# Performance work log

Measured on AMD Instinct MI355X. Metric: run time of the kernel, lower is better.

The kernel has to match this reference:

```python
import jax, jax.numpy as jnp
import numpy as np

D, H, DFF, K, S = 512, 8, 2048, 4, 4
DH = D // H
SHAPES = [(56, 56), (28, 28), (14, 14), (7, 7)]
B = 4


def setup_inputs() -> dict:
    key = jax.random.key(0)
    ks = jax.random.split(key, 32)
    inp = {}
    for i, (hl, wl) in enumerate(SHAPES):
        inp[f'src{i}'] = jax.random.normal(ks[i], (B, hl, wl, D), jnp.float32)
        inp[f'ref{i}'] = jax.random.uniform(ks[4 + i], (B, hl, wl, 2), jnp.float32)
    def lin(k, fan_in, fan_out):
        return jax.random.normal(k, (fan_in, fan_out), jnp.float32) * (1.0 / np.sqrt(fan_in))
    inp['Wv'] = lin(ks[8], D, D)
    inp['bv'] = jnp.zeros((D,), jnp.float32)
    inp['Woff'] = jax.random.normal(ks[9], (D, H * S * K * 2), jnp.float32) * 0.01
    inp['boff'] = jax.random.normal(ks[10], (H * S * K * 2,), jnp.float32) * 0.1
    inp['Wattn'] = jax.random.normal(ks[11], (D, H * S * K), jnp.float32) * 0.01
    inp['battn'] = jnp.zeros((H * S * K,), jnp.float32)
    inp['Wo'] = lin(ks[12], D, D)
    inp['bo'] = jnp.zeros((D,), jnp.float32)
    inp['W1'] = lin(ks[13], D, DFF)
    inp['b1'] = jnp.zeros((DFF,), jnp.float32)
    inp['W2'] = lin(ks[14], DFF, D)
    inp['b2'] = jnp.zeros((D,), jnp.float32)
    inp['g1'] = jnp.ones((D,), jnp.float32)
    inp['be1'] = jnp.zeros((D,), jnp.float32)
    inp['g2'] = jnp.ones((D,), jnp.float32)
    inp['be2'] = jnp.zeros((D,), jnp.float32)
    return inp


def layernorm(x, g, b, eps=1e-5):
    mu = jnp.mean(x, axis=-1, keepdims=True)
    var = jnp.mean(jnp.square(x - mu), axis=-1, keepdims=True)
    return (x - mu) * jax.lax.rsqrt(var + eps) * g + b


def bilinear_sample(value, loc):
    # value: [B, Hl, Wl, H, DH] per-scale projected values; loc: [B, Lq, H, K, 2] in [0,1]
    b, hl, wl, h, dh = value.shape
    x = loc[..., 0] * wl - 0.5
    y = loc[..., 1] * hl - 0.5
    x0f = jnp.floor(x); y0f = jnp.floor(y)
    wx1 = x - x0f; wx0 = 1.0 - wx1
    wy1 = y - y0f; wy0 = 1.0 - wy1
    x0 = x0f.astype(jnp.int32); y0 = y0f.astype(jnp.int32)
    vflat = value.transpose(0, 3, 1, 2, 4).reshape(b, h, hl * wl, dh)  # [B,H,HW,DH]

    def corner(xi, yi, w):
        valid = ((xi >= 0) & (xi < wl) & (yi >= 0) & (yi < hl)).astype(value.dtype)
        idx = jnp.clip(yi, 0, hl - 1) * wl + jnp.clip(xi, 0, wl - 1)  # [B,Lq,H,K]
        idx = idx.transpose(0, 2, 1, 3)  # [B,H,Lq,K]
        lq, kk = idx.shape[2], idx.shape[3]
        g = jnp.take_along_axis(vflat, idx.reshape(b, h, lq * kk)[..., None], axis=2)
        g = g.reshape(b, h, lq, kk, dh)
        wv = (w * valid).transpose(0, 2, 1, 3)[..., None]  # [B,H,Lq,K,1]
        return g * wv

    out = (corner(x0, y0, wx0 * wy0) + corner(x0 + 1, y0, wx1 * wy0)
           + corner(x0, y0 + 1, wx0 * wy1) + corner(x0 + 1, y0 + 1, wx1 * wy1))
    return out.transpose(0, 2, 1, 3, 4)  # [B,Lq,H,K,DH]


def _forward(src0, src1, src2, src3, ref0, ref1, ref2, ref3,
             Wv, bv, Woff, boff, Wattn, battn, Wo, bo, W1, b1, W2, b2, g1, be1, g2, be2):
    srcs = [src0, src1, src2, src3]
    refs = [ref0, ref1, ref2, ref3]
    # shared value projection per scale, split into heads
    values = [(s @ Wv + bv).reshape(s.shape[0], s.shape[1], s.shape[2], H, DH) for s in srcs]
    outs = []
    for src_l, ref_l in zip(srcs, refs):
        b = src_l.shape[0]
        q = src_l.reshape(b, -1, D)          # [B,Lq,D]
        ref = ref_l.reshape(b, -1, 2)        # [B,Lq,2]
        lq = q.shape[1]
        off = (q @ Woff + boff).reshape(b, lq, H, S, K, 2)
        attn = jax.nn.softmax((q @ Wattn + battn).reshape(b, lq, H, S * K), axis=-1)
        attn = attn.reshape(b, lq, H, S, K)
        acc = jnp.zeros((b, lq, H, DH), q.dtype)
        for li, (v, (hl, wl)) in enumerate(zip(values, SHAPES)):
            scale = jnp.array([wl, hl], q.dtype)
            loc = ref[:, :, None, None, :] + off[:, :, :, li] / scale  # [B,Lq,H,K,2]
            samp = bilinear_sample(v, loc)                              # [B,Lq,H,K,DH]
            acc = acc + jnp.einsum('blhk,blhkd->blhd', attn[:, :, :, li], samp)
        a = acc.reshape(b, lq, D) @ Wo + bo
        x = layernorm(q + a, g1, be1)
        f = jax.nn.relu(x @ W1 + b1) @ W2 + b2
        x = layernorm(x + f, g2, be2)
        outs.append(x)
    return jnp.concatenate(outs, axis=1)  # [B, sum(Hl*Wl), D]


def reference(src0, src1, src2, src3, ref0, ref1, ref2, ref3,
              Wv, bv, Woff, boff, Wattn, battn, Wo, bo, W1, b1, W2, b2, g1, be1, g2, be2):
    return _forward(src0, src1, src2, src3, ref0, ref1, ref2, ref3,
                    Wv, bv, Woff, boff, Wattn, battn, Wo, bo, W1, b1, W2, b2, g1, be1, g2, be2)
```

## Files before the change

### kernel.cpp

```cpp
#include <hip/hip_runtime.h>
#include <math.h>


#define TTOT 16660
#define TPAD 16768
#define LQTOT 4165

typedef __attribute__((ext_vector_type(8))) short bf16x8;
typedef __attribute__((ext_vector_type(4))) float f32x4;

typedef __attribute__((address_space(1))) const unsigned int g_u32;
typedef __attribute__((address_space(3))) unsigned int l_u32;

__device__ __forceinline__ unsigned short f2bf(float f) {
    unsigned u = __builtin_bit_cast(unsigned, f);
    u += 0x7fffu + ((u >> 16) & 1u);
    return (unsigned short)(u >> 16);
}
__device__ __forceinline__ float bf2f(unsigned short s) {
    unsigned u = ((unsigned)s) << 16;
    return __builtin_bit_cast(float, u);
}

__device__ __forceinline__ int permute_row(int t) {
    int off, area, qoff;
    if (t < 12544)      { off = 0;     area = 3136; qoff = 0;    }
    else if (t < 15680) { off = 12544; area = 784;  qoff = 3136; }
    else if (t < 16464) { off = 15680; area = 196;  qoff = 3920; }
    else                { off = 16464; area = 49;   qoff = 4116; }
    int rel = t - off;
    int b = rel / area;
    int pos = rel - b * area;
    return b * LQTOT + qoff + pos;
}

__device__ __forceinline__ const float* src_row(int row, const float* s0, const float* s1,
                                                const float* s2, const float* s3) {
    if (row < 12544) return s0 + (size_t)row * 512;
    if (row < 15680) return s1 + (size_t)(row - 12544) * 512;
    if (row < 16464) return s2 + (size_t)(row - 15680) * 512;
    return s3 + (size_t)(row - 16464) * 512;
}

__device__ __forceinline__ void async_copy16(const unsigned short* g, unsigned short* lds_wave_uniform) {
    __builtin_amdgcn_global_load_lds((g_u32*)g, (l_u32*)lds_wave_uniform, 16, 0, 0);
}

enum { EPI_SPLIT = 0, EPI_RESID_SRC = 1, EPI_RELU = 2, EPI_RESID_SCATTER = 3 };

struct GemmArgs {
    const unsigned short* A;
    const unsigned short* Bt;
    const float* bias0; const float* bias1; const float* bias2;
    const unsigned short* residb;
    const float* s0; const float* s1; const float* s2; const float* s3;
    void* out0; unsigned short* out1; unsigned short* out2;
    int M, N, Kd;
};

template <int EPI>
__global__ __launch_bounds__(256) void gemm_mfma(GemmArgs a)
{
    __shared__ unsigned short As[128 * 32];
    __shared__ unsigned short Bs[128 * 32];
    const int tid  = threadIdx.x;
    const int wave = tid >> 6;
    const int lane = tid & 63;
    const int m0 = blockIdx.y * 128;
    const int n0 = blockIdx.x * 128;

    const int srow = tid >> 2;
    const int kg   = (tid & 3) ^ ((tid >> 3) & 3);
    const unsigned short* Ag = a.A  + (size_t)(m0 + srow) * a.Kd + kg * 8;
    const unsigned short* Bg = a.Bt + (size_t)(n0 + srow) * a.Kd + kg * 8;
    const size_t rstep = (size_t)64 * a.Kd;
    unsigned short* ldsA0 = As + wave * 512;
    unsigned short* ldsA1 = As + 2048 + wave * 512;
    unsigned short* ldsB0 = Bs + wave * 512;
    unsigned short* ldsB1 = Bs + 2048 + wave * 512;

    const int wm = (wave >> 1) << 6;
    const int wn = (wave & 1) << 6;
    const int fm = lane & 15;
    const int fq = lane >> 4;
    const int slot = (fq ^ ((fm >> 1) & 3)) << 3;

    const f32x4 fzero = {0.f, 0.f, 0.f, 0.f};
    f32x4 acc[4][4];
#pragma unroll
    for (int i = 0; i < 4; ++i)
#pragma unroll
        for (int j = 0; j < 4; ++j) acc[i][j] = fzero;

    for (int k0 = 0; k0 < a.Kd; k0 += 32) {
        __syncthreads();
        async_copy16(Ag + k0,         ldsA0);
        async_copy16(Ag + rstep + k0, ldsA1);
        async_copy16(Bg + k0,         ldsB0);
        async_copy16(Bg + rstep + k0, ldsB1);
        __syncthreads();
        bf16x8 af[4], bfr[4];
#pragma unroll
        for (int mt = 0; mt < 4; ++mt)
            af[mt] = *(const bf16x8*)&As[(wm + mt * 16 + fm) * 32 + slot];
#pragma unroll
        for (int nt = 0; nt < 4; ++nt)
            bfr[nt] = *(const bf16x8*)&Bs[(wn + nt * 16 + fm) * 32 + slot];
#pragma unroll
        for (int mt = 0; mt < 4; ++mt)
#pragma unroll
            for (int nt = 0; nt < 4; ++nt)
                acc[mt][nt] = __builtin_amdgcn_mfma_f32_16x16x32_bf16(
                    af[mt], bfr[nt], acc[mt][nt], 0, 0, 0);
    }

    const int cn0 = n0 + wn + fm;
    int cols[4]; float bi[4];
#pragma unroll
    for (int nt = 0; nt < 4; ++nt) {
        const int c = cn0 + nt * 16;
        cols[nt] = c;
        if (EPI == EPI_SPLIT)
            bi[nt] = (c < 512) ? a.bias0[c] : (c < 768) ? a.bias1[c - 512] : a.bias2[c - 768];
        else
            bi[nt] = a.bias0[c];
    }
#pragma unroll
    for (int mt = 0; mt < 4; ++mt) {
#pragma unroll
        for (int r = 0; r < 4; ++r) {
            const int row = m0 + wm + mt * 16 + fq * 4 + r;
            if (row >= a.M) continue;
            const size_t ro = (size_t)row;
            const float* srcres = (EPI == EPI_RESID_SRC)
                                  ? src_row(row, a.s0, a.s1, a.s2, a.s3) : nullptr;
#pragma unroll
            for (int nt = 0; nt < 4; ++nt) {
                float v = acc[mt][nt][r] + bi[nt];
                const int c = cols[nt];
                if (EPI == EPI_SPLIT) {
                    if (c < 512)      ((unsigned short*)a.out0)[ro * 512 + c]        = f2bf(v);
                    else if (c < 768) a.out1[ro * 256 + (c - 512)]                   = f2bf(v);
                    else              a.out2[ro * 128 + (c - 768)]                   = f2bf(v);
                } else if (EPI == EPI_RESID_SRC) {
                    v += srcres[c];
                    ((unsigned short*)a.out0)[ro * 512 + c] = f2bf(v);
                } else if (EPI == EPI_RELU) {
                    v = fmaxf(v, 0.f);
                    ((unsigned short*)a.out0)[ro * 2048 + c] = f2bf(v);
                } else {
                    v += bf2f(a.residb[ro * 512 + c]);
                    ((float*)a.out0)[(size_t)permute_row(row) * 512 + c] = v;
                }
            }
        }
    }
}

__global__ __launch_bounds__(256) void transpose_bf16(
    const float* __restrict__ W, unsigned short* __restrict__ Wt, int K, int N)
{
    __shared__ unsigned short t[32][33];
    const int tx = threadIdx.x & 31, ty = threadIdx.x >> 5;
    const int nb = blockIdx.x * 32, kb = blockIdx.y * 32;
#pragma unroll
    for (int j = 0; j < 32; j += 8)
        t[ty + j][tx] = f2bf(W[(size_t)(kb + ty + j) * N + nb + tx]);
    __syncthreads();
#pragma unroll
    for (int j = 0; j < 32; j += 8)
        Wt[(size_t)(nb + ty + j) * K + kb + tx] = t[tx][ty + j];
}

__global__ __launch_bounds__(256) void concat_q_bf16(
    const float* __restrict__ s0, const float* __restrict__ s1,
    const float* __restrict__ s2, const float* __restrict__ s3,
    unsigned short* __restrict__ Qb)
{
    const int gid = blockIdx.x * 256 + threadIdx.x;
    if (gid >= TTOT * 128) return;
    const int e = gid * 4;
    const int row = e >> 9, col = e & 511;
    const float* sr = src_row(row, s0, s1, s2, s3);
    const float4 v = *(const float4*)(sr + col);
    ushort4 o;
    o.x = f2bf(v.x); o.y = f2bf(v.y); o.z = f2bf(v.z); o.w = f2bf(v.w);
    *(ushort4*)(Qb + (size_t)row * 512 + col) = o;
}

__global__ __launch_bounds__(256) void sample_attn(
    const unsigned short* __restrict__ Vp, const unsigned short* __restrict__ OFFB,
    const unsigned short* __restrict__ ATT,
    const float* __restrict__ rf0, const float* __restrict__ rf1,
    const float* __restrict__ rf2, const float* __restrict__ rf3,
    unsigned short* __restrict__ ACCb)
{
    __shared__ int   midx[4][16][4];
    __shared__ float mw[4][16][4];
    const int wave = threadIdx.x >> 6;
    const int lane = threadIdx.x & 63;
    const int wid  = (blockIdx.x << 2) + wave;
    const int t = wid >> 3;
    const int h = wid & 7;

    int soff, area;
    const float* rp;
    if (t < 12544)      { soff = 0;     area = 3136; rp = rf0 + (size_t)t * 2; }
    else if (t < 15680) { soff = 12544; area = 784;  rp = rf1 + (size_t)(t - 12544) * 2; }
    else if (t < 16464) { soff = 15680; area = 196;  rp = rf2 + (size_t)(t - 15680) * 2; }
    else                { soff = 16464; area = 49;   rp = rf3 + (size_t)(t - 16464) * 2; }
    const int b = (t - soff) / area;

    float sumv = 0.f;
    if (lane < 16) {
        const int s = lane;
        const int li = s >> 2;
        float logit = bf2f(ATT[(size_t)t * 128 + h * 16 + s]);
        float mx = logit;
#pragma unroll
        for (int o = 8; o > 0; o >>= 1) mx = fmaxf(mx, __shfl_xor(mx, o, 16));
        float e = __expf(logit - mx);
        sumv = e;
#pragma unroll
        for (int o = 8; o > 0; o >>= 1) sumv += __shfl_xor(sumv, o, 16);

        const int wl = 56 >> li;
        const int lvlbase = (li == 0) ? 0 : (li == 1) ? 12544 : (li == 2) ? 15680 : 16464;
        const int base = lvlbase + b * wl * wl;
        const float rx = rp[0], ry = rp[1];
        const float ox = bf2f(OFFB[(size_t)t * 256 + h * 32 + s * 2 + 0]);
        const float oy = bf2f(OFFB[(size_t)t * 256 + h * 32 + s * 2 + 1]);
        const float x = rx * (float)wl + ox - 0.5f;
        const float y = ry * (float)wl + oy - 0.5f;
        const float x0f = floorf(x), y0f = floorf(y);
        const float wx1 = x - x0f, wx0 = 1.f - wx1;
        const float wy1 = y - y0f, wy0 = 1.f - wy1;
        const int x0 = (int)x0f, y0 = (int)y0f;
        const int x1 = x0 + 1, y1 = y0 + 1;
        const int xc0 = min(max(x0, 0), wl - 1), xc1 = min(max(x1, 0), wl - 1);
        const int yc0 = min(max(y0, 0), wl - 1), yc1 = min(max(y1, 0), wl - 1);
        const float fx0 = (x0 >= 0 && x0 < wl) ? 1.f : 0.f;
        const float fx1 = (x1 >= 0 && x1 < wl) ? 1.f : 0.f;
        const float fy0 = (y0 >= 0 && y0 < wl) ? 1.f : 0.f;
        const float fy1 = (y1 >= 0 && y1 < wl) ? 1.f : 0.f;
        const int hb = h * 64;
        midx[wave][s][0] = (base + yc0 * wl + xc0) * 512 + hb;
        midx[wave][s][1] = (base + yc0 * wl + xc1) * 512 + hb;
        midx[wave][s][2] = (base + yc1 * wl + xc0) * 512 + hb;
        midx[wave][s][3] = (base + yc1 * wl + xc1) * 512 + hb;
        mw[wave][s][0] = wx0 * wy0 * fx0 * fy0 * e;
        mw[wave][s][1] = wx1 * wy0 * fx1 * fy0 * e;
        mw[wave][s][2] = wx0 * wy1 * fx0 * fy1 * e;
        mw[wave][s][3] = wx1 * wy1 * fx1 * fy1 * e;
    }
    __syncthreads();
    const float inv = 1.f / __shfl(sumv, 0, 64);

    float acc = 0.f;
#pragma unroll
    for (int s = 0; s < 16; ++s) {
        const int4  I = *(const int4*)&midx[wave][s][0];
        const float4 W = *(const float4*)&mw[wave][s][0];
        acc += W.x * bf2f(Vp[(size_t)(I.x + lane)]);
        acc += W.y * bf2f(Vp[(size_t)(I.y + lane)]);
        acc += W.z * bf2f(Vp[(size_t)(I.z + lane)]);
        acc += W.w * bf2f(Vp[(size_t)(I.w + lane)]);
    }
    ACCb[(size_t)t * 512 + h * 64 + lane] = f2bf(acc * inv);
}

__global__ __launch_bounds__(256) void ln_bf16(
    unsigned short* __restrict__ X, const float* __restrict__ g, const float* __restrict__ be)
{
    const int row = blockIdx.x;
    unsigned short* xr = X + (size_t)row * 512;
    const int tid = threadIdx.x;
    float v0 = bf2f(xr[tid]);
    float v1 = bf2f(xr[tid + 256]);
    float s = v0 + v1;
    float ss = v0 * v0 + v1 * v1;
#pragma unroll
    for (int o = 32; o > 0; o >>= 1) {
        s += __shfl_down(s, o, 64);
        ss += __shfl_down(ss, o, 64);
    }
    __shared__ float sm[4], sm2[4];
    const int w = tid >> 6;
    if ((tid & 63) == 0) { sm[w] = s; sm2[w] = ss; }
    __syncthreads();
    if (tid == 0) {
        sm[0] = sm[0] + sm[1] + sm[2] + sm[3];
        sm2[0] = sm2[0] + sm2[1] + sm2[2] + sm2[3];
    }
    __syncthreads();
    const float mu = sm[0] * (1.f / 512.f);
    const float var = sm2[0] * (1.f / 512.f) - mu * mu;
    const float rs = rsqrtf(var + 1e-5f);
    xr[tid]       = f2bf((v0 - mu) * rs * g[tid]       + be[tid]);
    xr[tid + 256] = f2bf((v1 - mu) * rs * g[tid + 256] + be[tid + 256]);
}

__global__ __launch_bounds__(256) void ln_f32(
    float* __restrict__ X, const float* __restrict__ g, const float* __restrict__ be)
{
    const int row = blockIdx.x;
    float* xr = X + (size_t)row * 512;
    const int tid = threadIdx.x;
    float v0 = xr[tid];
    float v1 = xr[tid + 256];
    float s = v0 + v1;
    float ss = v0 * v0 + v1 * v1;
#pragma unroll
    for (int o = 32; o > 0; o >>= 1) {
        s += __shfl_down(s, o, 64);
        ss += __shfl_down(ss, o, 64);
    }
    __shared__ float sm[4], sm2[4];
    const int w = tid >> 6;
    if ((tid & 63) == 0) { sm[w] = s; sm2[w] = ss; }
    __syncthreads();
    if (tid == 0) {
        sm[0] = sm[0] + sm[1] + sm[2] + sm[3];
        sm2[0] = sm2[0] + sm2[1] + sm2[2] + sm2[3];
    }
    __syncthreads();
    const float mu = sm[0] * (1.f / 512.f);
    const float var = sm2[0] * (1.f / 512.f) - mu * mu;
    const float rs = rsqrtf(var + 1e-5f);
    xr[tid]       = (v0 - mu) * rs * g[tid]       + be[tid];
    xr[tid + 256] = (v1 - mu) * rs * g[tid + 256] + be[tid + 256];
}

extern "C" void kernel_launch(void* const* d_in, const int* in_sizes, int n_in,
                              void* d_out, int out_size, void* d_ws, size_t ws_size,
                              hipStream_t stream)
{
    const float* src[4] = { (const float*)d_in[0], (const float*)d_in[2],
                            (const float*)d_in[4], (const float*)d_in[6] };
    const float* ref[4] = { (const float*)d_in[1], (const float*)d_in[3],
                            (const float*)d_in[5], (const float*)d_in[7] };
    const float* Wv    = (const float*)d_in[8];
    const float* bv    = (const float*)d_in[9];
    const float* Woff  = (const float*)d_in[10];
    const float* boff  = (const float*)d_in[11];
    const float* Wattn = (const float*)d_in[12];
    const float* battn = (const float*)d_in[13];
    const float* Wo    = (const float*)d_in[14];
    const float* bo    = (const float*)d_in[15];
    const float* W1    = (const float*)d_in[16];
    const float* b1    = (const float*)d_in[17];
    const float* W2    = (const float*)d_in[18];
    const float* b2    = (const float*)d_in[19];
    const float* g1    = (const float*)d_in[20];
    const float* be1   = (const float*)d_in[21];
    const float* g2    = (const float*)d_in[22];
    const float* be2   = (const float*)d_in[23];

    unsigned short* w    = (unsigned short*)d_ws;
    unsigned short* Qb   = w;
    unsigned short* Vp   = Qb   + (size_t)TPAD * 512;
    unsigned short* OFFB = Vp   + (size_t)TPAD * 512;
    unsigned short* ATT  = OFFB + (size_t)TPAD * 256;
    unsigned short* ACCb = ATT  + (size_t)TPAD * 128;
    unsigned short* X1b  = ACCb + (size_t)TPAD * 512;
    unsigned short* Fb   = X1b  + (size_t)TPAD * 512;
    unsigned short* Wcat = Fb   + (size_t)TPAD * 2048;
    unsigned short* Wot  = Wcat + (size_t)896 * 512;
    unsigned short* W1t  = Wot  + (size_t)512 * 512;
    unsigned short* W2t  = W1t  + (size_t)2048 * 512;

    const dim3 blk(256);

    transpose_bf16<<<dim3(16, 16), blk, 0, stream>>>(Wv,    Wcat,                    512, 512);
    transpose_bf16<<<dim3(8,  16), blk, 0, stream>>>(Woff,  Wcat + (size_t)512*512,  512, 256);
    transpose_bf16<<<dim3(4,  16), blk, 0, stream>>>(Wattn, Wcat + (size_t)768*512,  512, 128);
    transpose_bf16<<<dim3(16, 16), blk, 0, stream>>>(Wo,    Wot,                     512, 512);
    transpose_bf16<<<dim3(64, 16), blk, 0, stream>>>(W1,    W1t,                     512, 2048);
    transpose_bf16<<<dim3(16, 64), blk, 0, stream>>>(W2,    W2t,                     2048, 512);
    concat_q_bf16<<<dim3(8330), blk, 0, stream>>>(src[0], src[1], src[2], src[3], Qb);

    GemmArgs a1 = {};
    a1.A = Qb; a1.Bt = Wcat; a1.bias0 = bv; a1.bias1 = boff; a1.bias2 = battn;
    a1.out0 = Vp; a1.out1 = OFFB; a1.out2 = ATT; a1.M = TTOT; a1.N = 896; a1.Kd = 512;
    gemm_mfma<EPI_SPLIT><<<dim3(7, 131), blk, 0, stream>>>(a1);

    sample_attn<<<dim3(33320), blk, 0, stream>>>(Vp, OFFB, ATT,
                                                 ref[0], ref[1], ref[2], ref[3], ACCb);

    GemmArgs a2 = {};
    a2.A = ACCb; a2.Bt = Wot; a2.bias0 = bo;
    a2.s0 = src[0]; a2.s1 = src[1]; a2.s2 = src[2]; a2.s3 = src[3];
    a2.out0 = X1b; a2.M = TTOT; a2.N = 512; a2.Kd = 512;
    gemm_mfma<EPI_RESID_SRC><<<dim3(4, 131), blk, 0, stream>>>(a2);

    ln_bf16<<<dim3(TTOT), blk, 0, stream>>>(X1b, g1, be1);

    GemmArgs a3 = {};
    a3.A = X1b; a3.Bt = W1t; a3.bias0 = b1;
    a3.out0 = Fb; a3.M = TTOT; a3.N = 2048; a3.Kd = 512;
    gemm_mfma<EPI_RELU><<<dim3(16, 131), blk, 0, stream>>>(a3);

    GemmArgs a4 = {};
    a4.A = Fb; a4.Bt = W2t; a4.bias0 = b2; a4.residb = X1b;
    a4.out0 = d_out; a4.M = TTOT; a4.N = 512; a4.Kd = 2048;
    gemm_mfma<EPI_RESID_SCATTER><<<dim3(4, 131), blk, 0, stream>>>(a4);

    ln_f32<<<dim3(TTOT), blk, 0, stream>>>((float*)d_out, g2, be2);
}
```

Measured before the change: 473.2 us.

## Fuse prep kernels and widen sample_attn gathers to two heads per wave

Merges the six weight-transpose launches and the query concat into a single prep kernel dispatched by block index, which removes several kernel launches. sample_attn now runs one block per token, with each wave handling two heads. Each lane loads a packed pair of bf16 values with one 32-bit gather instead of a single 16-bit load. The softmax normalisation is folded into the per-sample weights, and the offset pair is read with one load. This halves the number of gather instructions and the grid size, at the cost of more setup lanes per wave.

Result: faster. 423.9 us (-10.4%).

```diff
diff --git a/kernel.cpp b/kernel.cpp
--- a/kernel.cpp
+++ b/kernel.cpp
@@ -20,6 +20,12 @@
 __device__ __forceinline__ float bf2f(unsigned short s) {
     unsigned u = ((unsigned)s) << 16;
     return __builtin_bit_cast(float, u);
+}
+__device__ __forceinline__ float bflo(unsigned u) {
+    return __builtin_bit_cast(float, u << 16);
+}
+__device__ __forceinline__ float bfhi(unsigned u) {
+    return __builtin_bit_cast(float, u & 0xffff0000u);
 }
 
 __device__ __forceinline__ int permute_row(int t) {
@@ -157,35 +163,46 @@
     }
 }
 
-__global__ __launch_bounds__(256) void transpose_bf16(
-    const float* __restrict__ W, unsigned short* __restrict__ Wt, int K, int N)
+struct PrepArgs {
+    const float *Wv, *Woff, *Wattn, *Wo, *W1, *W2;
+    unsigned short *Wcat, *Wot, *W1t, *W2t;
+    const float *s0, *s1, *s2, *s3;
+    unsigned short* Qb;
+};
+
+__global__ __launch_bounds__(256) void prep(PrepArgs p)
 {
     __shared__ unsigned short t[32][33];
-    const int tx = threadIdx.x & 31, ty = threadIdx.x >> 5;
-    const int nb = blockIdx.x * 32, kb = blockIdx.y * 32;
-#pragma unroll
-    for (int j = 0; j < 32; j += 8)
-        t[ty + j][tx] = f2bf(W[(size_t)(kb + ty + j) * N + nb + tx]);
-    __syncthreads();
-#pragma unroll
-    for (int j = 0; j < 32; j += 8)
-        Wt[(size_t)(nb + ty + j) * K + kb + tx] = t[tx][ty + j];
-}
-
-__global__ __launch_bounds__(256) void concat_q_bf16(
-    const float* __restrict__ s0, const float* __restrict__ s1,
-    const float* __restrict__ s2, const float* __restrict__ s3,
-    unsigned short* __restrict__ Qb)
-{
-    const int gid = blockIdx.x * 256 + threadIdx.x;
-    if (gid >= TTOT * 128) return;
-    const int e = gid * 4;
-    const int row = e >> 9, col = e & 511;
-    const float* sr = src_row(row, s0, s1, s2, s3);
-    const float4 v = *(const float4*)(sr + col);
-    ushort4 o;
-    o.x = f2bf(v.x); o.y = f2bf(v.y); o.z = f2bf(v.z); o.w = f2bf(v.w);
-    *(ushort4*)(Qb + (size_t)row * 512 + col) = o;
+    const int bid = blockIdx.x;
+    if (bid < 2752) {
+        const float* W; unsigned short* Wt; int K, N, lbx, rel;
+        if (bid < 256)       { W = p.Wv;    Wt = p.Wcat;                   K = 512;  N = 512;  lbx = 4; rel = bid; }
+        else if (bid < 384)  { W = p.Woff;  Wt = p.Wcat + (size_t)512*512; K = 512;  N = 256;  lbx = 3; rel = bid - 256; }
+        else if (bid < 448)  { W = p.Wattn; Wt = p.Wcat + (size_t)768*512; K = 512;  N = 128;  lbx = 2; rel = bid - 384; }
+        else if (bid < 704)  { W = p.Wo;    Wt = p.Wot;                    K = 512;  N = 512;  lbx = 4; rel = bid - 448; }
+        else if (bid < 1728) { W = p.W1;    Wt = p.W1t;                    K = 512;  N = 2048; lbx = 6; rel = bid - 704; }
+        else                 { W = p.W2;    Wt = p.W2t;                    K = 2048; N = 512;  lbx = 4; rel = bid - 1728; }
+        const int bx = rel & ((1 << lbx) - 1);
+        const int by = rel >> lbx;
+        const int tx = threadIdx.x & 31, ty = threadIdx.x >> 5;
+        const int nb = bx * 32, kb = by * 32;
+#pragma unroll
+        for (int j = 0; j < 32; j += 8)
+            t[ty + j][tx] = f2bf(W[(size_t)(kb + ty + j) * N + nb + tx]);
+        __syncthreads();
+#pragma unroll
+        for (int j = 0; j < 32; j += 8)
+            Wt[(size_t)(nb + ty + j) * K + kb + tx] = t[tx][ty + j];
+    } else {
+        const int gid = (bid - 2752) * 256 + threadIdx.x;
+        const int e = gid * 4;
+        const int row = e >> 9, col = e & 511;
+        const float* sr = src_row(row, p.s0, p.s1, p.s2, p.s3);
+        const float4 v = *(const float4*)(sr + col);
+        ushort4 o;
+        o.x = f2bf(v.x); o.y = f2bf(v.y); o.z = f2bf(v.z); o.w = f2bf(v.w);
+        *(ushort4*)(p.Qb + (size_t)row * 512 + col) = o;
+    }
 }
 
 __global__ __launch_bounds__(256) void sample_attn(
@@ -195,13 +212,12 @@
     const float* __restrict__ rf2, const float* __restrict__ rf3,
     unsigned short* __restrict__ ACCb)
 {
-    __shared__ int   midx[4][16][4];
-    __shared__ float mw[4][16][4];
+    __shared__ int   midx[4][2][16][4];
+    __shared__ float mw[4][2][16][4];
     const int wave = threadIdx.x >> 6;
     const int lane = threadIdx.x & 63;
-    const int wid  = (blockIdx.x << 2) + wave;
-    const int t = wid >> 3;
-    const int h = wid & 7;
+    const int t  = blockIdx.x;
+    const int hp = wave;
 
     int soff, area;
     const float* rp;
@@ -211,25 +227,28 @@
     else                { soff = 16464; area = 49;   rp = rf3 + (size_t)(t - 16464) * 2; }
     const int b = (t - soff) / area;
 
-    float sumv = 0.f;
-    if (lane < 16) {
-        const int s = lane;
+    if (lane < 32) {
+        const int hl = lane >> 4;
+        const int s  = lane & 15;
+        const int h  = hp * 2 + hl;
         const int li = s >> 2;
         float logit = bf2f(ATT[(size_t)t * 128 + h * 16 + s]);
         float mx = logit;
 #pragma unroll
         for (int o = 8; o > 0; o >>= 1) mx = fmaxf(mx, __shfl_xor(mx, o, 16));
         float e = __expf(logit - mx);
-        sumv = e;
+        float sumv = e;
 #pragma unroll
         for (int o = 8; o > 0; o >>= 1) sumv += __shfl_xor(sumv, o, 16);
+        const float ew = e / sumv;
 
         const int wl = 56 >> li;
         const int lvlbase = (li == 0) ? 0 : (li == 1) ? 12544 : (li == 2) ? 15680 : 16464;
         const int base = lvlbase + b * wl * wl;
         const float rx = rp[0], ry = rp[1];
-        const float ox = bf2f(OFFB[(size_t)t * 256 + h * 32 + s * 2 + 0]);
-        const float oy = bf2f(OFFB[(size_t)t * 256 + h * 32 + s * 2 + 1]);
+        const unsigned off2 = *(const unsigned*)(OFFB + (size_t)t * 256 + h * 32 + s * 2);
+        const float ox = bflo(off2);
+        const float oy = bfhi(off2);
         const float x = rx * (float)wl + ox - 0.5f;
         const float y = ry * (float)wl + oy - 0.5f;
         const float x0f = floorf(x), y0f = floorf(y);
@@ -243,30 +262,40 @@
         const float fx1 = (x1 >= 0 && x1 < wl) ? 1.f : 0.f;
         const float fy0 = (y0 >= 0 && y0 < wl) ? 1.f : 0.f;
         const float fy1 = (y1 >= 0 && y1 < wl) ? 1.f : 0.f;
-        const int hb = h * 64;
-        midx[wave][s][0] = (base + yc0 * wl + xc0) * 512 + hb;
-        midx[wave][s][1] = (base + yc0 * wl + xc1) * 512 + hb;
-        midx[wave][s][2] = (base + yc1 * wl + xc0) * 512 + hb;
-        midx[wave][s][3] = (base + yc1 * wl + xc1) * 512 + hb;
-        mw[wave][s][0] = wx0 * wy0 * fx0 * fy0 * e;
-        mw[wave][s][1] = wx1 * wy0 * fx1 * fy0 * e;
-        mw[wave][s][2] = wx0 * wy1 * fx0 * fy1 * e;
-        mw[wave][s][3] = wx1 * wy1 * fx1 * fy1 * e;
+        const int hb2 = h * 128;
+        midx[wave][hl][s][0] = (base + yc0 * wl + xc0) * 1024 + hb2;
+        midx[wave][hl][s][1] = (base + yc0 * wl + xc1) * 1024 + hb2;
+        midx[wave][hl][s][2] = (base + yc1 * wl + xc0) * 1024 + hb2;
+        midx[wave][hl][s][3] = (base + yc1 * wl + xc1) * 1024 + hb2;
+        mw[wave][hl][s][0] = wx0 * wy0 * fx0 * fy0 * ew;
+        mw[wave][hl][s][1] = wx1 * wy0 * fx1 * fy0 * ew;
+        mw[wave][hl][s][2] = wx0 * wy1 * fx0 * fy1 * ew;
+        mw[wave][hl][s][3] = wx1 * wy1 * fx1 * fy1 * ew;
     }
     __syncthreads();
-    const float inv = 1.f / __shfl(sumv, 0, 64);
-
-    float acc = 0.f;
+
+    const int hl = lane >> 5;
+    const int laneoff = (lane & 31) * 4;
+    const char* vb = (const char*)Vp;
+    float accL = 0.f, accH = 0.f;
 #pragma unroll
     for (int s = 0; s < 16; ++s) {
-        const int4  I = *(const int4*)&midx[wave][s][0];
-        const float4 W = *(const float4*)&mw[wave][s][0];
-        acc += W.x * bf2f(Vp[(size_t)(I.x + lane)]);
-        acc += W.y * bf2f(Vp[(size_t)(I.y + lane)]);
-        acc += W.z * bf2f(Vp[(size_t)(I.z + lane)]);
-        acc += W.w * bf2f(Vp[(size_t)(I.w + lane)]);
-    }
-    ACCb[(size_t)t * 512 + h * 64 + lane] = f2bf(acc * inv);
+        const int4   I = *(const int4*)&midx[wave][hl][s][0];
+        const float4 W = *(const float4*)&mw[wave][hl][s][0];
+        const unsigned u0 = *(const unsigned*)(vb + (I.x + laneoff));
+        const unsigned u1 = *(const unsigned*)(vb + (I.y + laneoff));
+        const unsigned u2 = *(const unsigned*)(vb + (I.z + laneoff));
+        const unsigned u3 = *(const unsigned*)(vb + (I.w + laneoff));
+        accL += W.x * bflo(u0); accH += W.x * bfhi(u0);
+        accL += W.y * bflo(u1); accH += W.y * bfhi(u1);
+        accL += W.z * bflo(u2); accH += W.z * bfhi(u2);
+        accL += W.w * bflo(u3); accH += W.w * bfhi(u3);
+    }
+    const int h = hp * 2 + hl;
+    ushort2 o;
+    o.x = f2bf(accL);
+    o.y = f2bf(accH);
+    *(ushort2*)((char*)ACCb + (size_t)t * 1024 + h * 128 + laneoff) = o;
 }
 
 __global__ __launch_bounds__(256) void ln_bf16(
@@ -371,21 +400,20 @@
 
     const dim3 blk(256);
 
-    transpose_bf16<<<dim3(16, 16), blk, 0, stream>>>(Wv,    Wcat,                    512, 512);
-    transpose_bf16<<<dim3(8,  16), blk, 0, stream>>>(Woff,  Wcat + (size_t)512*512,  512, 256);
-    transpose_bf16<<<dim3(4,  16), blk, 0, stream>>>(Wattn, Wcat + (size_t)768*512,  512, 128);
-    transpose_bf16<<<dim3(16, 16), blk, 0, stream>>>(Wo,    Wot,                     512, 512);
-    transpose_bf16<<<dim3(64, 16), blk, 0, stream>>>(W1,    W1t,                     512, 2048);
-    transpose_bf16<<<dim3(16, 64), blk, 0, stream>>>(W2,    W2t,                     2048, 512);
-    concat_q_bf16<<<dim3(8330), blk, 0, stream>>>(src[0], src[1], src[2], src[3], Qb);
+    PrepArgs pp = {};
+    pp.Wv = Wv; pp.Woff = Woff; pp.Wattn = Wattn; pp.Wo = Wo; pp.W1 = W1; pp.W2 = W2;
+    pp.Wcat = Wcat; pp.Wot = Wot; pp.W1t = W1t; pp.W2t = W2t;
+    pp.s0 = src[0]; pp.s1 = src[1]; pp.s2 = src[2]; pp.s3 = src[3];
+    pp.Qb = Qb;
+    prep<<<dim3(11082), blk, 0, stream>>>(pp);
 
     GemmArgs a1 = {};
     a1.A = Qb; a1.Bt = Wcat; a1.bias0 = bv; a1.bias1 = boff; a1.bias2 = battn;
     a1.out0 = Vp; a1.out1 = OFFB; a1.out2 = ATT; a1.M = TTOT; a1.N = 896; a1.Kd = 512;
     gemm_mfma<EPI_SPLIT><<<dim3(7, 131), blk, 0, stream>>>(a1);
 
-    sample_attn<<<dim3(33320), blk, 0, stream>>>(Vp, OFFB, ATT,
-                                                 ref[0], ref[1], ref[2], ref[3], ACCb);
+    sample_attn<<<dim3(TTOT), blk, 0, stream>>>(Vp, OFFB, ATT,
+                                                ref[0], ref[1], ref[2], ref[3], ACCb);
 
     GemmArgs a2 = {};
     a2.A = ACCb; a2.Bt = Wot; a2.bias0 = bo;
```
